# Kernel tuning notes

Measured on AMD Instinct MI355X. Metric: run time of the kernel, lower is better.

## Reference

```python
import jax, jax.numpy as jnp
import numpy as np

N, M, D, DV = 8192, 8192, 128, 128

def setup_inputs() -> dict:
    key = jax.random.key(0)
    kq, kk, kv = jax.random.split(key, 3)
    return {
        "Q": jax.random.normal(kq, (N, D), dtype=jnp.float32),
        "K": jax.random.normal(kk, (M, D), dtype=jnp.float32),
        "V": jax.random.normal(kv, (M, DV), dtype=jnp.float32),
    }

def reference(Q, K, V):
    # scores: [N, M] = Q @ K^T (no 1/sqrt(d) scaling, matching the source)
    scores = jnp.einsum("nd,md->nm", Q, K)
    attention_weights = jax.nn.softmax(scores, axis=1)  # softmax over keys
    return jnp.einsum("nm,mv->nv", attention_weights, V)  # [N, DV]
```

## Files before the change

kernel.cpp:

```cpp
#include <hip/hip_runtime.h>
#include <hip/hip_bf16.h>

#define NQ   8192
#define NKEY 8192
#define DH   128

#define BQ   128
#define BK   32
#define BUFB 16384
#define LOG2E 1.44269504088896340736f

typedef __attribute__((ext_vector_type(8)))  short    short8;
typedef __attribute__((ext_vector_type(4)))  short    short4v;
typedef _Float16 half8 __attribute__((ext_vector_type(8)));
typedef __attribute__((ext_vector_type(16))) float    f32x16;
typedef __attribute__((ext_vector_type(4)))  float    float4v;

union BFU { __hip_bfloat16 b; unsigned short u; };
__device__ __forceinline__ unsigned short f2bf(float x) { BFU u; u.b = __float2bfloat16(x); return u.u; }

__device__ __forceinline__ void full_drain_barrier() {
    __builtin_amdgcn_s_waitcnt(0);
    __syncthreads();
}

__global__ void prep(const float* __restrict__ K, const float* __restrict__ V,
                     _Float16* __restrict__ Kh, unsigned short* __restrict__ Vt) {
    __shared__ __attribute__((aligned(16))) unsigned short tile[64 * 72];
    int b = blockIdx.x;
    int t = threadIdx.x;
    if (b < 512) {
        int idx = (b * 256 + t) * 8;
        float4v x0 = *(const float4v*)(K + idx);
        float4v x1 = *(const float4v*)(K + idx + 4);
        half8 o;
#pragma unroll
        for (int j = 0; j < 4; ++j) { o[j] = (_Float16)x0[j]; o[4 + j] = (_Float16)x1[j]; }
        *(half8*)(Kh + idx) = o;
    } else {
        int tv = b - 512;
        int m0 = (tv >> 1) * 64, n0 = (tv & 1) * 64;
#pragma unroll
        for (int it = 0; it < 4; ++it) {
            int id = t + it * 256;
            int mm = id >> 4, nn0 = (id & 15) * 4;
            int mmP = (mm & ~12) | ((mm & 4) << 1) | ((mm & 8) >> 1);
            float4v x = *(const float4v*)(V + (size_t)(m0 + mm) * DH + n0 + nn0);
#pragma unroll
            for (int j = 0; j < 4; ++j)
                tile[(nn0 + j) * 72 + mmP] = f2bf(x[j]);
        }
        __syncthreads();
        int nn = t >> 2, ch = t & 3;
        *(short8*)(Vt + (size_t)(n0 + nn) * NKEY + m0 + ch * 16)     = *(const short8*)&tile[nn * 72 + ch * 16];
        *(short8*)(Vt + (size_t)(n0 + nn) * NKEY + m0 + ch * 16 + 8) = *(const short8*)&tile[nn * 72 + ch * 16 + 8];
    }
}

__launch_bounds__(256, 2)
__global__ void attn_fwd(const float* __restrict__ Q,
                         const _Float16* __restrict__ Kh,
                         const unsigned short* __restrict__ Vt,
                         unsigned short* __restrict__ Opart, float* __restrict__ lpart,
                         float* __restrict__ out, int KS) {
    __shared__ __attribute__((aligned(16))) char sbuf[2 * BUFB];

    const int tid  = threadIdx.x;
    const int lane = tid & 63;
    const int w    = tid >> 6;
    const int l31  = lane & 31;
    const int h    = lane >> 5;

    const int s  = blockIdx.x % KS;
    const int qb = blockIdx.x / KS;
    const int mlen   = NKEY / KS;
    const int kbase  = s * mlen;
    const int ntiles = mlen / BK;

    const char* gbase[4]; int mult[4]; int ldsoff[4];
#pragma unroll
    for (int i = 0; i < 4; ++i) {
        int Lb = w * 256 + i * 64;
        int L  = Lb + lane;
        const char* gb; int mu;
        if (Lb < 512) {
            int r = L >> 4, ck = (L & 15) ^ (r & 15);
            gb = (const char*)Kh + r * 256 + ck * 16; mu = 256;
        } else {
            int Lv = L - 512; int n = Lv >> 2;
            int cv = (Lv & 3) ^ (n & 3) ^ ((n >> 2) & 3);
            gb = (const char*)Vt + (size_t)n * (NKEY * 2) + cv * 16; mu = 2;
        }
        gbase[i] = gb; mult[i] = mu; ldsoff[i] = Lb * 16;
    }

    const int qrow = qb * BQ + w * 32 + l31;
    half8 qf[8];
#pragma unroll
    for (int c = 0; c < 8; ++c) {
        const float* qp = Q + (size_t)qrow * DH + c * 16 + h * 8;
        float4v x0 = *(const float4v*)qp;
        float4v x1 = *(const float4v*)(qp + 4);
#pragma unroll
        for (int i = 0; i < 4; ++i) {
            qf[c][i]     = (_Float16)(x0[i] * LOG2E);
            qf[c][4 + i] = (_Float16)(x1[i] * LOG2E);
        }
    }

    int koff[8];
#pragma unroll
    for (int c = 0; c < 8; ++c)
        koff[c] = l31 * 256 + (((c * 2 + h) ^ (l31 & 15)) << 4);
    int vsw[2];
#pragma unroll
    for (int kg = 0; kg < 2; ++kg)
        vsw[kg] = 8192 + l31 * 64 + (((kg * 2 + h) ^ (l31 & 3) ^ ((l31 >> 2) & 3)) << 4);

    float lsum = 0.0f;
    f32x16 O[4];
#pragma unroll
    for (int ct = 0; ct < 4; ++ct)
#pragma unroll
        for (int r = 0; r < 16; ++r) O[ct][r] = 0.0f;

    auto stage = [&](int t, int bufbyte) {
        int kb = kbase + t * BK;
#pragma unroll
        for (int i = 0; i < 4; ++i) {
            const char* g = gbase[i] + (size_t)kb * mult[i];
            __builtin_amdgcn_global_load_lds(
                (const __attribute__((address_space(1))) unsigned int*)g,
                (__attribute__((address_space(3))) unsigned int*)(sbuf + bufbyte + ldsoff[i]),
                16, 0, 0);
        }
    };

    auto compute_tile = [&](int BUF) {
        const char* bp = sbuf + BUF;
        f32x16 S;
#pragma unroll
        for (int r = 0; r < 16; ++r) S[r] = 0.0f;
#pragma unroll
        for (int c = 0; c < 8; ++c) {
            half8 kf = *(const half8*)(bp + koff[c]);
            S = __builtin_amdgcn_mfma_f32_32x32x16_f16(kf, qf[c], S, 0, 0, 0);
        }
        float p[16]; float ps = 0.0f;
#pragma unroll
        for (int r = 0; r < 16; ++r) { p[r] = __builtin_amdgcn_exp2f(S[r]); ps += p[r]; }
        ps += __shfl_xor(ps, 32, 64);
        lsum += ps;
        union PU { unsigned int u[4]; short8 s8; } B[2];
#pragma unroll
        for (int j = 0; j < 4; ++j) {
            B[0].u[j] = __builtin_amdgcn_perm(__float_as_uint(p[2*j+1]), __float_as_uint(p[2*j]),   0x07060302u);
            B[1].u[j] = __builtin_amdgcn_perm(__float_as_uint(p[2*j+9]), __float_as_uint(p[2*j+8]), 0x07060302u);
        }
#pragma unroll
        for (int ct = 0; ct < 4; ++ct) {
#pragma unroll
            for (int kg = 0; kg < 2; ++kg) {
                short8 va = *(const short8*)(bp + ct * 2048 + vsw[kg]);
                O[ct] = __builtin_amdgcn_mfma_f32_32x32x16_bf16(va, B[kg].s8, O[ct], 0, 0, 0);
            }
        }
    };

    stage(0, 0);
    for (int t = 0; t < ntiles; t += 2) {
        full_drain_barrier();
        stage(t + 1, BUFB);
        compute_tile(0);
        full_drain_barrier();
        if (t + 2 < ntiles) stage(t + 2, 0);
        compute_tile(BUFB);
    }

    {
        unsigned short* Ob = Opart + ((size_t)s * NQ + qrow) * DH;
#pragma unroll
        for (int ct = 0; ct < 4; ++ct)
#pragma unroll
            for (int g = 0; g < 4; ++g) {
                short4v v;
#pragma unroll
                for (int j = 0; j < 4; ++j) v[j] = (short)f2bf(O[ct][4 * g + j]);
                *(short4v*)(Ob + ct * 32 + 8 * g + 4 * h) = v;
            }
        if (h == 0)
            lpart[(size_t)s * NQ + qrow] = lsum;
    }
}

__global__ void attn_combine(const unsigned short* __restrict__ Opart,
                             const float* __restrict__ lpart, float* __restrict__ out, int KS) {
    int idx = blockIdx.x * 256 + threadIdx.x;
    int row = idx >> 5;
    int col = (idx & 31) << 2;
    float den = 0.0f;
    float a0 = 0.0f, a1 = 0.0f, a2 = 0.0f, a3 = 0.0f;
    for (int s2 = 0; s2 < KS; ++s2) {
        den += lpart[(size_t)s2 * NQ + row];
        const unsigned short* op = Opart + ((size_t)s2 * NQ + row) * DH + col;
        uint2 u = *(const uint2*)op;
        a0 += __uint_as_float(u.x << 16);
        a1 += __uint_as_float(u.x & 0xffff0000u);
        a2 += __uint_as_float(u.y << 16);
        a3 += __uint_as_float(u.y & 0xffff0000u);
    }
    float r = 1.0f / den;
    float4v v; v[0] = a0 * r; v[1] = a1 * r; v[2] = a2 * r; v[3] = a3 * r;
    *(float4v*)(out + (size_t)row * DH + col) = v;
}

extern "C" void kernel_launch(void* const* d_in, const int* in_sizes, int n_in,
                              void* d_out, int out_size, void* d_ws, size_t ws_size,
                              hipStream_t stream) {
    const float* Q = (const float*)d_in[0];
    const float* K = (const float*)d_in[1];
    const float* V = (const float*)d_in[2];
    float* out = (float*)d_out;

    const size_t prep_bytes = 2 * (size_t)NKEY * DH * sizeof(unsigned short);
    int KS = 16;
    while (KS > 1 &&
           ws_size < prep_bytes + (size_t)KS * ((size_t)NQ * DH * 2 + NQ * 4))
        KS >>= 1;

    _Float16* Kh = (_Float16*)d_ws;
    unsigned short* Vt = (unsigned short*)(Kh + (size_t)NKEY * DH);
    unsigned short* Opart = Vt + (size_t)NKEY * DH;
    float* lpart = (float*)(Opart + (size_t)KS * NQ * DH);

    hipLaunchKernelGGL(prep, dim3(768), dim3(256), 0, stream, K, V, Kh, Vt);
    hipLaunchKernelGGL(attn_fwd, dim3((NQ / BQ) * KS), dim3(256), 0, stream,
                       Q, Kh, Vt, Opart, lpart, out, KS);
    hipLaunchKernelGGL(attn_combine, dim3((NQ * DH) / 4 / 256), dim3(256), 0, stream,
                       Opart, lpart, out, KS);
}
```

Baseline: 122.5 us.

## Split output columns across wave pairs to halve per-wave accumulators and raise occupancy

Each block now covers 64 query rows instead of 128, and pairs of waves share the same 32 rows. Each wave of a pair accumulates half of the 128 output columns, so every wave keeps two accumulator tiles instead of four. That cuts register use, which allows a launch bound of 4 blocks per CU, and the key split is reduced from 16 to 8 chunks, which shrinks the partial-sum write and combine traffic. The trade-off is that both waves of a pair recompute the same QK^T scores and exponentials, doubling that work, and K/V tiles are reloaded for twice as many query blocks.

```diff
diff --git a/kernel.cpp b/kernel.cpp
--- a/kernel.cpp
+++ b/kernel.cpp
@@ -5,7 +5,7 @@
 #define NKEY 8192
 #define DH   128
 
-#define BQ   128
+#define BQ   64
 #define BK   32
 #define BUFB 16384
 #define LOG2E 1.44269504088896340736f
@@ -57,7 +57,7 @@
     }
 }
 
-__launch_bounds__(256, 2)
+__launch_bounds__(256, 4)
 __global__ void attn_fwd(const float* __restrict__ Q,
                          const _Float16* __restrict__ Kh,
                          const unsigned short* __restrict__ Vt,
@@ -70,6 +70,8 @@
     const int w    = tid >> 6;
     const int l31  = lane & 31;
     const int h    = lane >> 5;
+    const int g    = w >> 1;
+    const int d    = w & 1;
 
     const int s  = blockIdx.x % KS;
     const int qb = blockIdx.x / KS;
@@ -94,7 +96,7 @@
         gbase[i] = gb; mult[i] = mu; ldsoff[i] = Lb * 16;
     }
 
-    const int qrow = qb * BQ + w * 32 + l31;
+    const int qrow = qb * BQ + g * 32 + l31;
     half8 qf[8];
 #pragma unroll
     for (int c = 0; c < 8; ++c) {
@@ -118,19 +120,19 @@
         vsw[kg] = 8192 + l31 * 64 + (((kg * 2 + h) ^ (l31 & 3) ^ ((l31 >> 2) & 3)) << 4);
 
     float lsum = 0.0f;
-    f32x16 O[4];
-#pragma unroll
-    for (int ct = 0; ct < 4; ++ct)
-#pragma unroll
-        for (int r = 0; r < 16; ++r) O[ct][r] = 0.0f;
+    f32x16 O[2];
+#pragma unroll
+    for (int ci = 0; ci < 2; ++ci)
+#pragma unroll
+        for (int r = 0; r < 16; ++r) O[ci][r] = 0.0f;
 
     auto stage = [&](int t, int bufbyte) {
         int kb = kbase + t * BK;
 #pragma unroll
         for (int i = 0; i < 4; ++i) {
-            const char* g = gbase[i] + (size_t)kb * mult[i];
+            const char* gp = gbase[i] + (size_t)kb * mult[i];
             __builtin_amdgcn_global_load_lds(
-                (const __attribute__((address_space(1))) unsigned int*)g,
+                (const __attribute__((address_space(1))) unsigned int*)gp,
                 (__attribute__((address_space(3))) unsigned int*)(sbuf + bufbyte + ldsoff[i]),
                 16, 0, 0);
         }
@@ -149,7 +151,6 @@
         float p[16]; float ps = 0.0f;
 #pragma unroll
         for (int r = 0; r < 16; ++r) { p[r] = __builtin_amdgcn_exp2f(S[r]); ps += p[r]; }
-        ps += __shfl_xor(ps, 32, 64);
         lsum += ps;
         union PU { unsigned int u[4]; short8 s8; } B[2];
 #pragma unroll
@@ -158,11 +159,12 @@
             B[1].u[j] = __builtin_amdgcn_perm(__float_as_uint(p[2*j+9]), __float_as_uint(p[2*j+8]), 0x07060302u);
         }
 #pragma unroll
-        for (int ct = 0; ct < 4; ++ct) {
+        for (int ci = 0; ci < 2; ++ci) {
+            int ct = 2 * d + ci;
 #pragma unroll
             for (int kg = 0; kg < 2; ++kg) {
                 short8 va = *(const short8*)(bp + ct * 2048 + vsw[kg]);
-                O[ct] = __builtin_amdgcn_mfma_f32_32x32x16_bf16(va, B[kg].s8, O[ct], 0, 0, 0);
+                O[ci] = __builtin_amdgcn_mfma_f32_32x32x16_bf16(va, B[kg].s8, O[ci], 0, 0, 0);
             }
         }
     };
@@ -177,18 +179,21 @@
         compute_tile(BUFB);
     }
 
+    lsum += __shfl_xor(lsum, 32, 64);
     {
         unsigned short* Ob = Opart + ((size_t)s * NQ + qrow) * DH;
 #pragma unroll
-        for (int ct = 0; ct < 4; ++ct)
-#pragma unroll
-            for (int g = 0; g < 4; ++g) {
+        for (int ci = 0; ci < 2; ++ci) {
+            int ct = 2 * d + ci;
+#pragma unroll
+            for (int g2 = 0; g2 < 4; ++g2) {
                 short4v v;
 #pragma unroll
-                for (int j = 0; j < 4; ++j) v[j] = (short)f2bf(O[ct][4 * g + j]);
-                *(short4v*)(Ob + ct * 32 + 8 * g + 4 * h) = v;
+                for (int j = 0; j < 4; ++j) v[j] = (short)f2bf(O[ci][4 * g2 + j]);
+                *(short4v*)(Ob + ct * 32 + 8 * g2 + 4 * h) = v;
             }
-        if (h == 0)
+        }
+        if (d == 0 && h == 0)
             lpart[(size_t)s * NQ + qrow] = lsum;
     }
 }
@@ -223,7 +228,7 @@
     float* out = (float*)d_out;
 
     const size_t prep_bytes = 2 * (size_t)NKEY * DH * sizeof(unsigned short);
-    int KS = 16;
+    int KS = 8;
     while (KS > 1 &&
            ws_size < prep_bytes + (size_t)KS * ((size_t)NQ * DH * 2 + NQ * 4))
         KS >>= 1;
```

After: 137.0 us. +11.8%, slower.
